# Kernel optimization log

Measured on AMD Instinct MI355X. Metric: run time of the kernel, lower is better.

Reference implementation:

```python
import jax, jax.numpy as jnp
import numpy as np

H = 256   # hidden_dim
C = 512   # num_classes (HMM states)
V = 32000 # vocab
N = 64    # batch
T = 512   # sequence length


def _res_layer(x, w1, b1, w2, b2):
    # compound-PCFG ResLayer: x + relu(lin2(relu(lin1(x))))
    return x + jax.nn.relu(jax.nn.relu(x @ w1 + b1) @ w2 + b2)


def _mlp_res2(x, res_w, res_b):
    # res_w: [2,2,H,H], res_b: [2,2,H] -> two stacked ResLayers
    for i in range(2):
        x = _res_layer(x, res_w[i, 0], res_b[i, 0], res_w[i, 1], res_b[i, 1])
    return x


def setup_inputs() -> dict:
    key = jax.random.key(0)
    ks = jax.random.split(key, 12)
    s = 1.0 / np.sqrt(H)  # xavier-ish scale
    return {
        "text": jax.random.randint(ks[0], (N, T), 0, V, dtype=jnp.int32),
        "start_emb": jax.random.normal(ks[1], (H,), jnp.float32),
        "start_w": jax.random.normal(ks[2], (H, H), jnp.float32) * s,
        "start_b": jnp.zeros((H,), jnp.float32),
        "start_res_w": jax.random.normal(ks[3], (2, 2, H, H), jnp.float32) * s,
        "start_res_b": jnp.zeros((2, 2, H), jnp.float32),
        "state_emb": jax.random.normal(ks[4], (C, H), jnp.float32) * s,
        "next_state_emb": jax.random.normal(ks[5], (C, H), jnp.float32) * s,
        "preterminal_emb": jax.random.normal(ks[6], (C, H), jnp.float32) * s,
        "term_res_w": jax.random.normal(ks[7], (2, 2, H, H), jnp.float32) * s,
        "term_res_b": jnp.zeros((2, 2, H), jnp.float32),
        "terminal_emb": jax.random.normal(ks[8], (V, H), jnp.float32) * s,
    }


def reference(text, start_emb, start_w, start_b, start_res_w, start_res_b,
              state_emb, next_state_emb, preterminal_emb,
              term_res_w, term_res_b, terminal_emb):
    # --- start distribution: start_mlp(start_emb) @ next_state_emb.T (tie_start) ---
    fx = start_emb @ start_w + start_b          # Linear
    fx = _mlp_res2(fx, start_res_w, start_res_b)
    start = jax.nn.log_softmax(fx @ next_state_emb.T, axis=-1)       # [C]

    # --- transition: state_emb @ next_state_emb.T, row log-softmax ---
    transition = jax.nn.log_softmax(state_emb @ next_state_emb.T, axis=-1)  # [C,C]

    # --- emission: terminal_mlp(preterminal_emb) @ terminal_emb.T ---
    fe = _mlp_res2(preterminal_emb, term_res_w, term_res_b)           # [C,H]
    emission = jax.nn.log_softmax(fe @ terminal_emb.T, axis=-1)       # [C,V]

    # --- HMM forward algorithm (log-space scan over time) ---
    em_tok = emission.T[text]                 # [N,T,C] log p(x_t | z_t=c)
    alpha0 = start[None, :] + em_tok[:, 0]    # [N,C]

    def step(alpha, e_t):
        # alpha: [N,C]; logsumexp over previous state
        alpha = jax.nn.logsumexp(alpha[:, :, None] + transition[None], axis=1) + e_t
        return alpha, None

    alpha_T, _ = jax.lax.scan(step, alpha0, jnp.swapaxes(em_tok, 0, 1)[1:])
    evidence = jax.nn.logsumexp(alpha_T, axis=-1).sum()
    return evidence
```

## Files before the change

### kernel.cpp

```cpp
#include <hip/hip_runtime.h>
#include <hip/hip_bf16.h>

#define HD 256
#define CD 512
#define VD 32000
#define ND 64
#define TD 512

typedef __attribute__((ext_vector_type(8))) short short8;
typedef __attribute__((ext_vector_type(4))) float floatx4;
typedef __attribute__((ext_vector_type(8))) int int32x8;

__device__ inline float bf2f(unsigned short u) {
  union { unsigned u; float f; } t; t.u = ((unsigned)u) << 16; return t.f;
}
__device__ inline unsigned short f2bf(float x) {
  union { float f; unsigned u; } t; t.f = x;
  unsigned u = t.u;
  u += 0x7FFFu + ((u >> 16) & 1u);
  return (unsigned short)(u >> 16);
}
__device__ inline float bf_lo(unsigned u) { union { unsigned u; float f; } t; t.u = u << 16; return t.f; }
__device__ inline float bf_hi(unsigned u) { union { unsigned u; float f; } t; t.u = u & 0xFFFF0000u; return t.f; }

__device__ inline floatx4 zf4() { floatx4 v; v[0] = v[1] = v[2] = v[3] = 0.f; return v; }
__device__ inline floatx4 mfma16(short8 a, short8 b, floatx4 c) {
  return __builtin_amdgcn_mfma_f32_16x16x32_bf16(a, b, c, 0, 0, 0);
}
__device__ inline floatx4 mfma_mx(int32x8 a, int32x8 b, floatx4 c) {
  return __builtin_amdgcn_mfma_scale_f32_16x16x128_f8f6f4(
      a, b, c, 0, 0, 0, 0x7F7F7F7F, 0, 0x7F7F7F7F);
}

__global__ void k_sm(const float* __restrict__ emb, const float* __restrict__ W,
                     const float* __restrict__ bb, const float* __restrict__ s_rw,
                     const float* __restrict__ s_rb, const float* __restrict__ nextE,
                     float* __restrict__ startO,
                     const float* __restrict__ pretE, const float* __restrict__ t_rw,
                     const float* __restrict__ t_rb, float* __restrict__ fe) {
  __shared__ float x[HD], h[HD];
  __shared__ float lg[2 * HD];
  __shared__ float red[8];
  const int j = threadIdx.x;
  if (blockIdx.x != 0) {
    const int row = blockIdx.x - 1;
    x[j] = pretE[row * HD + j];
    __syncthreads();
    for (int L = 0; L < 2; ++L) {
      const float* w1 = t_rw + (size_t)(L * 2 + 0) * HD * HD;
      const float* b1 = t_rb + (L * 2 + 0) * HD;
      const float* w2 = t_rw + (size_t)(L * 2 + 1) * HD * HD;
      const float* b2 = t_rb + (L * 2 + 1) * HD;
      float a = b1[j];
#pragma unroll 4
      for (int i = 0; i < HD; ++i) a += x[i] * w1[i * HD + j];
      a = fmaxf(a, 0.f);
      h[j] = a;
      __syncthreads();
      float o = b2[j];
#pragma unroll 4
      for (int i = 0; i < HD; ++i) o += h[i] * w2[i * HD + j];
      o = x[j] + fmaxf(o, 0.f);
      __syncthreads();
      x[j] = o;
      __syncthreads();
    }
    fe[row * HD + j] = x[j];
    return;
  }
  x[j] = emb[j];
  __syncthreads();
  float a = bb[j];
#pragma unroll 8
  for (int i = 0; i < HD; ++i) a += x[i] * W[i * HD + j];
  __syncthreads();
  x[j] = a;
  __syncthreads();
  for (int L = 0; L < 2; ++L) {
    const float* w1 = s_rw + (size_t)(L * 2 + 0) * HD * HD;
    const float* b1 = s_rb + (L * 2 + 0) * HD;
    const float* w2 = s_rw + (size_t)(L * 2 + 1) * HD * HD;
    const float* b2 = s_rb + (L * 2 + 1) * HD;
    float t = b1[j];
#pragma unroll 8
    for (int i = 0; i < HD; ++i) t += x[i] * w1[i * HD + j];
    t = fmaxf(t, 0.f);
    h[j] = t;
    __syncthreads();
    float o = b2[j];
#pragma unroll 8
    for (int i = 0; i < HD; ++i) o += h[i] * w2[i * HD + j];
    o = x[j] + fmaxf(o, 0.f);
    __syncthreads();
    x[j] = o;
    __syncthreads();
  }
  {
    const int w = j >> 6, l = j & 63;
    for (int rr = w * 128; rr < (w + 1) * 128; ++rr) {
      float s = 0.f;
#pragma unroll
      for (int k = 0; k < 4; ++k) s += x[l + k * 64] * nextE[rr * HD + l + k * 64];
#pragma unroll
      for (int off = 32; off >= 1; off >>= 1) s += __shfl_down(s, off);
      if (l == 0) lg[rr] = s;
    }
  }
  __syncthreads();
  float lg0 = lg[j], lg1 = lg[j + 256];
  float m = fmaxf(lg0, lg1);
#pragma unroll
  for (int sh = 1; sh <= 32; sh <<= 1) m = fmaxf(m, __shfl_xor(m, sh));
  if ((j & 63) == 0) red[j >> 6] = m;
  __syncthreads();
  m = fmaxf(fmaxf(red[0], red[1]), fmaxf(red[2], red[3]));
  __syncthreads();
  float s = __expf(lg0 - m) + __expf(lg1 - m);
#pragma unroll
  for (int sh = 1; sh <= 32; sh <<= 1) s += __shfl_xor(s, sh);
  if ((j & 63) == 0) red[j >> 6] = s;
  __syncthreads();
  s = red[0] + red[1] + red[2] + red[3];
  float ls = __logf(s);
  startO[j] = lg0 - m - ls;
  startO[j + 256] = lg1 - m - ls;
}

#define GEMM_LDS (2 * 128 * 528)
__global__ __launch_bounds__(512) void k_gemm2(const float* __restrict__ A0,
                                               const float* __restrict__ B0,
                                               unsigned short* __restrict__ out0,
                                               const float* __restrict__ A1,
                                               const float* __restrict__ B1,
                                               unsigned short* __restrict__ out1) {
  extern __shared__ char smem[];
  char* sA = smem;
  char* sB = smem + 128 * 528;
  const int tid = threadIdx.x;
  const int bx = blockIdx.x;
  const float* A; const float* B; unsigned short* out; int mbase;
  if (bx < 250) { A = A0; B = B0; out = out0; mbase = bx * 128; }
  else          { A = A1; B = B1; out = out1; mbase = (bx - 250) * 128; }
  const int row = tid >> 2, seg = tid & 3;
  {
    const float4* srcA = (const float4*)(A + (size_t)(mbase + row) * HD + seg * 64);
    uint2* dA = (uint2*)(sA + row * 528 + seg * 128);
#pragma unroll
    for (int i = 0; i < 16; ++i) {
      float4 va = srcA[i];
      dA[i] = make_uint2((unsigned)f2bf(va.x) | ((unsigned)f2bf(va.y) << 16),
                         (unsigned)f2bf(va.z) | ((unsigned)f2bf(va.w) << 16));
    }
  }
  const int w = tid >> 6, l = tid & 63, l15 = l & 15, quad = l >> 4;
  const char* arow = sA + (w * 16 + l15) * 528 + quad * 16;
  const char* brow = sB + l15 * 528 + quad * 16;
  for (int ny = 0; ny < 4; ++ny) {
    __syncthreads();
    {
      const float4* srcB = (const float4*)(B + (size_t)(ny * 128 + row) * HD + seg * 64);
      uint2* dB = (uint2*)(sB + row * 528 + seg * 128);
#pragma unroll
      for (int i = 0; i < 16; ++i) {
        float4 vb = srcB[i];
        dB[i] = make_uint2((unsigned)f2bf(vb.x) | ((unsigned)f2bf(vb.y) << 16),
                           (unsigned)f2bf(vb.z) | ((unsigned)f2bf(vb.w) << 16));
      }
    }
    __syncthreads();
    floatx4 acc[8];
#pragma unroll
    for (int nt = 0; nt < 8; ++nt) acc[nt] = zf4();
#pragma unroll
    for (int kc = 0; kc < 8; ++kc) {
      short8 a = *(const short8*)(arow + kc * 64);
#pragma unroll
      for (int nt = 0; nt < 8; ++nt) {
        short8 b = *(const short8*)(brow + nt * 16 * 528 + kc * 64);
        acc[nt] = mfma16(a, b, acc[nt]);
      }
    }
#pragma unroll
    for (int nt = 0; nt < 8; ++nt)
#pragma unroll
      for (int r = 0; r < 4; ++r) {
        int m = mbase + w * 16 + quad * 4 + r;
        int n = ny * 128 + nt * 16 + l15;
        out[(size_t)m * CD + n] = f2bf(acc[nt][r]);
      }
  }
}

__global__ __launch_bounds__(512) void k_sml(const unsigned short* __restrict__ tlg,
                                             unsigned char* __restrict__ P8,
                                             unsigned char* __restrict__ PT8,
                                             const unsigned short* __restrict__ logT,
                                             float* __restrict__ part,
                                             float* __restrict__ lse,
                                             unsigned int* __restrict__ cnt) {
  __shared__ float red[8];
  __shared__ int s_last;
  const int tid = threadIdx.x;
  if (blockIdx.x < 512) {
    const int row = blockIdx.x;
    float v = bf2f(tlg[row * CD + tid]);
    float m = v;
#pragma unroll
    for (int sh = 1; sh <= 32; sh <<= 1) m = fmaxf(m, __shfl_xor(m, sh));
    if ((tid & 63) == 0) red[tid >> 6] = m;
    __syncthreads();
    m = fmaxf(fmaxf(fmaxf(red[0], red[1]), fmaxf(red[2], red[3])),
              fmaxf(fmaxf(red[4], red[5]), fmaxf(red[6], red[7])));
    __syncthreads();
    float e = __expf(v - m);
    float s = e;
#pragma unroll
    for (int sh = 1; sh <= 32; sh <<= 1) s += __shfl_xor(s, sh);
    if ((tid & 63) == 0) red[tid >> 6] = s;
    __syncthreads();
    s = red[0] + red[1] + red[2] + red[3] + red[4] + red[5] + red[6] + red[7];
    float inv = 512.0f / s;
    int b0 = __builtin_amdgcn_cvt_pk_fp8_f32(e * inv, e * inv, 0, false);
    unsigned char byte = (unsigned char)(b0 & 0xff);
    P8[row * CD + tid] = byte;
    PT8[(size_t)tid * CD + row] = byte;
    return;
  }
  const int b = blockIdx.x - 512, c = tid;
  {
    const unsigned short* p = logT + (size_t)b * 256 * CD + c;
    float m = -1e30f, s = 0.f;
    for (int i = 0; i < 256; ++i) {
      float v = bf2f(p[(size_t)i * CD]);
      float nm = fmaxf(m, v);
      s = s * __expf(m - nm) + __expf(v - nm);
      m = nm;
    }
    part[b * 1024 + c] = m;
    part[b * 1024 + 512 + c] = s;
  }
  __threadfence();
  if (tid == 0) s_last = (atomicAdd(cnt, 1u) == 124u) ? 1 : 0;
  __syncthreads();
  if (s_last) {
    __threadfence();
    float m = -1e30f, s = 0.f;
    for (int i = 0; i < 125; ++i) {
      float mi = part[i * 1024 + c], si = part[i * 1024 + 512 + c];
      float nm = fmaxf(m, mi);
      s = s * __expf(m - nm) + si * __expf(mi - nm);
      m = nm;
    }
    lse[c] = m + __logf(s);
  }
}

__global__ __launch_bounds__(512) void k_gather(const int* __restrict__ text,
                                                const unsigned short* __restrict__ logT,
                                                const float* __restrict__ lse,
                                                unsigned short* __restrict__ em) {
  const int b = blockIdx.x;
  const int g = b >> 8, t = b & 255;
  const int dir = g >> 2, q = g & 3;
  const int tg = dir ? (511 - t) : t;
  const int tid = threadIdx.x, w = tid >> 6, l = tid & 63;
  const int l15 = l & 15, quad = l >> 4;
  const int n = q * 16 + l15;
  const int tok = text[n * TD + tg];
  const unsigned short* row = logT + (size_t)tok * CD;
  unsigned outp[8];
#pragma unroll
  for (int nt = 0; nt < 4; ++nt) {
    int c0 = w * 64 + nt * 16 + quad * 4;
    uint2 rv = *(const uint2*)(row + c0);
    float4 ls = *(const float4*)(lse + c0);
    float E0 = __expf(bf_lo(rv.x) - ls.x);
    float E1 = __expf(bf_hi(rv.x) - ls.y);
    float E2 = __expf(bf_lo(rv.y) - ls.z);
    float E3 = __expf(bf_hi(rv.y) - ls.w);
    outp[nt * 2 + 0] = (unsigned)f2bf(E0) | ((unsigned)f2bf(E1) << 16);
    outp[nt * 2 + 1] = (unsigned)f2bf(E2) | ((unsigned)f2bf(E3) << 16);
  }
  uint4* dst = (uint4*)(em + (((size_t)b * 8 + w) * 64 + l) * 16);
  dst[0] = make_uint4(outp[0], outp[1], outp[2], outp[3]);
  dst[1] = make_uint4(outp[4], outp[5], outp[6], outp[7]);
}

__global__ __launch_bounds__(512, 2) void k_scan(const unsigned char* __restrict__ P8,
                                                 const unsigned char* __restrict__ PT8,
                                                 const unsigned short* __restrict__ em,
                                                 const float* __restrict__ startv,
                                                 float* __restrict__ alphaF,
                                                 float* __restrict__ alphaB,
                                                 unsigned int* __restrict__ cnt,
                                                 float* __restrict__ out) {
  __shared__ unsigned char Abuf[8 * 512];
  __shared__ float scratch[8 * 8];
  __shared__ int s_last;
  const int g = blockIdx.x, dir = g >> 3, q = g & 7;
  const int tid = threadIdx.x, w = tid >> 6, l = tid & 63;
  const int l15 = l & 15, quad = l >> 4;
  const int r7 = l15 & 7, sel = l15 >> 3;
  const int colbase = w * 64;
  const unsigned char* Pb = dir ? P8 : PT8;

  int32x8 Prf[4][4];
#pragma unroll
  for (int kc = 0; kc < 4; ++kc)
#pragma unroll
    for (int mt = 0; mt < 4; ++mt) {
      const uint4* p = (const uint4*)(Pb + (size_t)(colbase + mt * 16 + l15) * CD + kc * 128 + quad * 32);
      uint4 x0 = p[0], x1 = p[1];
      Prf[kc][mt] = (int32x8){(int)x0.x, (int)x0.y, (int)x0.z, (int)x0.w,
                              (int)x1.x, (int)x1.y, (int)x1.z, (int)x1.w};
    }

  unsigned char* wr0 = Abuf + r7 * 512 + (((w * 4 + sel * 2 + 0) ^ r7) << 4) + quad * 4;
  unsigned char* wr1 = Abuf + r7 * 512 + (((w * 4 + sel * 2 + 1) ^ r7) << 4) + quad * 4;
  const unsigned char* rdrow = Abuf + r7 * 512;

  const int go = dir * 4 + (q >> 1);
  const int o = quad * 16 + (q & 1) * 8 + r7;
  const unsigned short* emp = em + (((size_t)go * 256 * 8 + w) * 64 + o) * 16 + sel * 8;
  const size_t emstride = 8 * 64 * 16;

  float Msum = 0.f;
  const float LGA = 5.54517744f;
  const float LGP = 6.23832463f;
  const float LGAP = 11.78350207f;

  auto tail = [&](float* v, float sub) {
    float m = fmaxf(fmaxf(fmaxf(v[0], v[1]), fmaxf(v[2], v[3])),
                    fmaxf(fmaxf(v[4], v[5]), fmaxf(v[6], v[7])));
    m = fmaxf(m, __shfl_xor(m, 8));
    m = fmaxf(m, __shfl_xor(m, 16));
    m = fmaxf(m, __shfl_xor(m, 32));
    if (sel == 0 && quad == 0) scratch[r7 * 8 + w] = m;
    __syncthreads();
    const floatx4* sr = (const floatx4*)(scratch + r7 * 8);
    floatx4 s0 = sr[0], s1 = sr[1];
    m = fmaxf(fmaxf(fmaxf(s0[0], s0[1]), fmaxf(s0[2], s0[3])),
              fmaxf(fmaxf(s1[0], s1[1]), fmaxf(s1[2], s1[3])));
    float inv = __builtin_amdgcn_rcpf(m) * 256.0f;
    Msum += __logf(m) - sub;
    int pk0 = __builtin_amdgcn_cvt_pk_fp8_f32(v[0] * inv, v[1] * inv, 0, false);
    pk0 = __builtin_amdgcn_cvt_pk_fp8_f32(v[2] * inv, v[3] * inv, pk0, true);
    *(int*)wr0 = pk0;
    int pk1 = __builtin_amdgcn_cvt_pk_fp8_f32(v[4] * inv, v[5] * inv, 0, false);
    pk1 = __builtin_amdgcn_cvt_pk_fp8_f32(v[6] * inv, v[7] * inv, pk1, true);
    *(int*)wr1 = pk1;
    __syncthreads();
  };

  {
    uint4 e0 = *(const uint4*)emp;
    unsigned eu[4] = {e0.x, e0.y, e0.z, e0.w};
    float v[8];
#pragma unroll
    for (int i = 0; i < 2; ++i)
#pragma unroll
      for (int r = 0; r < 4; ++r) {
        int j = i * 4 + r;
        float E = (j & 1) ? bf_hi(eu[j >> 1]) : bf_lo(eu[j >> 1]);
        float st = dir ? 1.f : __expf(startv[colbase + (sel * 2 + i) * 16 + quad * 4 + r]);
        v[j] = st * E;
      }
    tail(v, LGA);
  }

  uint4 ec = *(const uint4*)(emp + emstride);
  const int nloop = dir ? 255 : 254;
  for (int s = 1; s <= nloop; ++s) {
    int32x8 bfr[4];
#pragma unroll
    for (int kc = 0; kc < 4; ++kc) {
      int u0 = kc * 8 + quad * 2;
      uint4 x0 = *(const uint4*)(rdrow + (((u0 + 0) ^ r7) << 4));
      uint4 x1 = *(const uint4*)(rdrow + (((u0 + 1) ^ r7) << 4));
      bfr[kc] = (int32x8){(int)x0.x, (int)x0.y, (int)x0.z, (int)x0.w,
                          (int)x1.x, (int)x1.y, (int)x1.z, (int)x1.w};
    }
    uint4 en = *(const uint4*)(emp + (size_t)(s + 1) * emstride);
    floatx4 acc[4];
#pragma unroll
    for (int mt = 0; mt < 4; ++mt) acc[mt] = zf4();
#pragma unroll
    for (int kc = 0; kc < 4; ++kc) {
      acc[0] = mfma_mx(Prf[kc][0], bfr[kc], acc[0]);
      acc[1] = mfma_mx(Prf[kc][1], bfr[kc], acc[1]);
      acc[2] = mfma_mx(Prf[kc][2], bfr[kc], acc[2]);
      acc[3] = mfma_mx(Prf[kc][3], bfr[kc], acc[3]);
    }
    unsigned eu[4] = {ec.x, ec.y, ec.z, ec.w};
    float v[8];
#pragma unroll
    for (int i = 0; i < 2; ++i)
#pragma unroll
      for (int r = 0; r < 4; ++r) {
        int j = i * 4 + r;
        float E = (j & 1) ? bf_hi(eu[j >> 1]) : bf_lo(eu[j >> 1]);
        float a0 = (i == 0) ? acc[0][r] : acc[1][r];
        float a1 = (i == 0) ? acc[2][r] : acc[3][r];
        v[j] = (sel ? a1 : a0) * E;
      }
    tail(v, LGAP);
    ec = en;
  }
  {
    int32x8 bfr[4];
#pragma unroll
    for (int kc = 0; kc < 4; ++kc) {
      int u0 = kc * 8 + quad * 2;
      uint4 x0 = *(const uint4*)(rdrow + (((u0 + 0) ^ r7) << 4));
      uint4 x1 = *(const uint4*)(rdrow + (((u0 + 1) ^ r7) << 4));
      bfr[kc] = (int32x8){(int)x0.x, (int)x0.y, (int)x0.z, (int)x0.w,
                          (int)x1.x, (int)x1.y, (int)x1.z, (int)x1.w};
    }
    floatx4 acc[4];
#pragma unroll
    for (int mt = 0; mt < 4; ++mt) acc[mt] = zf4();
#pragma unroll
    for (int kc = 0; kc < 4; ++kc) {
      acc[0] = mfma_mx(Prf[kc][0], bfr[kc], acc[0]);
      acc[1] = mfma_mx(Prf[kc][1], bfr[kc], acc[1]);
      acc[2] = mfma_mx(Prf[kc][2], bfr[kc], acc[2]);
      acc[3] = mfma_mx(Prf[kc][3], bfr[kc], acc[3]);
    }
    unsigned eu[4] = {ec.x, ec.y, ec.z, ec.w};
    float* dst = dir ? alphaB : alphaF;
#pragma unroll
    for (int i = 0; i < 2; ++i) {
      int mt0 = i, mt1 = 2 + i;
      float4 ov;
      float vv[4];
#pragma unroll
      for (int r = 0; r < 4; ++r) {
        int j = i * 4 + r;
        float E = dir ? 1.f : ((j & 1) ? bf_hi(eu[j >> 1]) : bf_lo(eu[j >> 1]));
        float a0 = acc[mt0][r];
        float a1 = acc[mt1][r];
        vv[r] = (sel ? a1 : a0) * E;
      }
      ov.x = __logf(vv[0]) + Msum - LGP;
      ov.y = __logf(vv[1]) + Msum - LGP;
      ov.z = __logf(vv[2]) + Msum - LGP;
      ov.w = __logf(vv[3]) + Msum - LGP;
      *(float4*)&dst[(size_t)(q * 8 + r7) * CD + colbase + (sel * 2 + i) * 16 + quad * 4] = ov;
    }
  }
  __threadfence();
  if (tid == 0) s_last = (atomicAdd(cnt, 1u) == 15u) ? 1 : 0;
  __syncthreads();
  if (s_last) {
    __threadfence();
    float ev = 0.f;
    for (int i = 0; i < 8; ++i) {
      int n = w * 8 + i;
      float x[8];
      float m = -1e30f;
#pragma unroll
      for (int k = 0; k < 8; ++k) {
        x[k] = alphaF[n * CD + k * 64 + l] + alphaB[n * CD + k * 64 + l];
        m = fmaxf(m, x[k]);
      }
#pragma unroll
      for (int sh = 1; sh <= 32; sh <<= 1) m = fmaxf(m, __shfl_xor(m, sh));
      float s = 0.f;
#pragma unroll
      for (int k = 0; k < 8; ++k) s += __expf(x[k] - m);
#pragma unroll
      for (int sh = 1; sh <= 32; sh <<= 1) s += __shfl_xor(s, sh);
      ev += m + __logf(s);
    }
    if (l == 0) scratch[w] = ev;
    __syncthreads();
    if (tid == 0) {
      float tot = 0.f;
      for (int i = 0; i < 8; ++i) tot += scratch[i];
      out[0] = tot;
    }
  }
}

extern "C" void kernel_launch(void* const* d_in, const int* in_sizes, int n_in,
                              void* d_out, int out_size, void* d_ws, size_t ws_size,
                              hipStream_t stream) {
  (void)in_sizes; (void)n_in; (void)out_size;
  const int* text = (const int*)d_in[0];
  const float* s_emb = (const float*)d_in[1];
  const float* s_w = (const float*)d_in[2];
  const float* s_b = (const float*)d_in[3];
  const float* s_rw = (const float*)d_in[4];
  const float* s_rb = (const float*)d_in[5];
  const float* stateE = (const float*)d_in[6];
  const float* nextE = (const float*)d_in[7];
  const float* pretE = (const float*)d_in[8];
  const float* t_rw = (const float*)d_in[9];
  const float* t_rb = (const float*)d_in[10];
  const float* termE = (const float*)d_in[11];
  float* out = (float*)d_out;

  char* ws = (char*)d_ws;
  size_t off = 0;
  auto alloc = [&](size_t bytes) {
    void* p = ws + off;
    off = (off + bytes + 255) & ~(size_t)255;
    return p;
  };
  unsigned int* w_cnt = (unsigned int*)alloc(256);
  float* w_start = (float*)alloc(CD * 4);
  unsigned short* w_tlg = (unsigned short*)alloc((size_t)CD * CD * 2);
  unsigned char* w_P8 = (unsigned char*)alloc((size_t)CD * CD);
  unsigned char* w_PT8 = (unsigned char*)alloc((size_t)CD * CD);
  float* w_fe = (float*)alloc((size_t)CD * HD * 4);
  unsigned short* w_logT = (unsigned short*)alloc((size_t)VD * CD * 2);
  float* w_part = (float*)alloc((size_t)125 * 1024 * 4);
  float* w_lse = (float*)alloc(CD * 4);
  unsigned short* w_em = (unsigned short*)alloc((size_t)8 * 256 * 512 * 16 * 2);
  float* w_aF = (float*)alloc((size_t)ND * CD * 4);
  float* w_aB = (float*)alloc((size_t)ND * CD * 4);
  if (off > ws_size) return;

  hipFuncSetAttribute(reinterpret_cast<const void*>(k_gemm2),
                      hipFuncAttributeMaxDynamicSharedMemorySize, GEMM_LDS);

  hipMemsetAsync(w_cnt, 0, 256, stream);

  k_sm<<<513, 256, 0, stream>>>(s_emb, s_w, s_b, s_rw, s_rb, nextE, w_start,
                                pretE, t_rw, t_rb, w_fe);
  k_gemm2<<<254, 512, GEMM_LDS, stream>>>(termE, w_fe, w_logT, stateE, nextE, w_tlg);
  k_sml<<<637, 512, 0, stream>>>(w_tlg, w_P8, w_PT8, w_logT, w_part, w_lse, w_cnt + 1);
  k_gather<<<2048, 512, 0, stream>>>(text, w_logT, w_lse, w_em);
  k_scan<<<16, 512, 0, stream>>>(w_P8, w_PT8, w_em, w_start, w_aF, w_aB, w_cnt, out);
}
```

Baseline: 608.3 us.

## Fuse emission gather into scan and use per-block MX scales instead of block-wide max

Removes the separate gather kernel. The scan kernel now loads token ids into LDS and computes the exponentiated emission values directly from logT and lse, one step ahead. Each wave now renormalizes with a power-of-two exponent taken from its own max. That exponent goes to LDS as an E8M0 scale byte, which the scaled MFMA consumes per K-chunk, so the cross-wave max reduction and one barrier per step are gone. The A buffer is double-buffered to allow this. The risks are more global-load latency on the serial scan path and precision changes from the fixed offsets and clamped scales.

```diff
diff --git a/kernel.cpp b/kernel.cpp
--- a/kernel.cpp
+++ b/kernel.cpp
@@ -27,9 +27,9 @@
 __device__ inline floatx4 mfma16(short8 a, short8 b, floatx4 c) {
   return __builtin_amdgcn_mfma_f32_16x16x32_bf16(a, b, c, 0, 0, 0);
 }
-__device__ inline floatx4 mfma_mx(int32x8 a, int32x8 b, floatx4 c) {
+__device__ inline floatx4 mfma_mxs(int32x8 a, int32x8 b, floatx4 c, unsigned sb) {
   return __builtin_amdgcn_mfma_scale_f32_16x16x128_f8f6f4(
-      a, b, c, 0, 0, 0, 0x7F7F7F7F, 0, 0x7F7F7F7F);
+      a, b, c, 0, 0, 0, 0x7F7F7F7F, 0, (int)sb);
 }
 
 __global__ void k_sm(const float* __restrict__ emb, const float* __restrict__ W,
@@ -255,53 +255,27 @@
   }
 }
 
-__global__ __launch_bounds__(512) void k_gather(const int* __restrict__ text,
-                                                const unsigned short* __restrict__ logT,
-                                                const float* __restrict__ lse,
-                                                unsigned short* __restrict__ em) {
-  const int b = blockIdx.x;
-  const int g = b >> 8, t = b & 255;
-  const int dir = g >> 2, q = g & 3;
-  const int tg = dir ? (511 - t) : t;
-  const int tid = threadIdx.x, w = tid >> 6, l = tid & 63;
-  const int l15 = l & 15, quad = l >> 4;
-  const int n = q * 16 + l15;
-  const int tok = text[n * TD + tg];
-  const unsigned short* row = logT + (size_t)tok * CD;
-  unsigned outp[8];
-#pragma unroll
-  for (int nt = 0; nt < 4; ++nt) {
-    int c0 = w * 64 + nt * 16 + quad * 4;
-    uint2 rv = *(const uint2*)(row + c0);
-    float4 ls = *(const float4*)(lse + c0);
-    float E0 = __expf(bf_lo(rv.x) - ls.x);
-    float E1 = __expf(bf_hi(rv.x) - ls.y);
-    float E2 = __expf(bf_lo(rv.y) - ls.z);
-    float E3 = __expf(bf_hi(rv.y) - ls.w);
-    outp[nt * 2 + 0] = (unsigned)f2bf(E0) | ((unsigned)f2bf(E1) << 16);
-    outp[nt * 2 + 1] = (unsigned)f2bf(E2) | ((unsigned)f2bf(E3) << 16);
-  }
-  uint4* dst = (uint4*)(em + (((size_t)b * 8 + w) * 64 + l) * 16);
-  dst[0] = make_uint4(outp[0], outp[1], outp[2], outp[3]);
-  dst[1] = make_uint4(outp[4], outp[5], outp[6], outp[7]);
-}
-
 __global__ __launch_bounds__(512, 2) void k_scan(const unsigned char* __restrict__ P8,
                                                  const unsigned char* __restrict__ PT8,
-                                                 const unsigned short* __restrict__ em,
+                                                 const unsigned short* __restrict__ logT,
+                                                 const float* __restrict__ lse,
+                                                 const int* __restrict__ text,
                                                  const float* __restrict__ startv,
                                                  float* __restrict__ alphaF,
                                                  float* __restrict__ alphaB,
                                                  unsigned int* __restrict__ cnt,
                                                  float* __restrict__ out) {
-  __shared__ unsigned char Abuf[8 * 512];
-  __shared__ float scratch[8 * 8];
+  __shared__ unsigned char Abuf[2 * 8 * 512];
+  __shared__ unsigned char Tbuf[2 * 128];
+  __shared__ int txtL[8 * 272];
+  __shared__ float scr[8];
   __shared__ int s_last;
   const int g = blockIdx.x, dir = g >> 3, q = g & 7;
   const int tid = threadIdx.x, w = tid >> 6, l = tid & 63;
   const int l15 = l & 15, quad = l >> 4;
   const int r7 = l15 & 7, sel = l15 >> 3;
   const int colbase = w * 64;
+  const int c0 = colbase + sel * 32 + quad * 4;
   const unsigned char* Pb = dir ? P8 : PT8;
 
   int32x8 Prf[4][4];
@@ -315,62 +289,94 @@
                               (int)x1.x, (int)x1.y, (int)x1.z, (int)x1.w};
     }
 
-  unsigned char* wr0 = Abuf + r7 * 512 + (((w * 4 + sel * 2 + 0) ^ r7) << 4) + quad * 4;
-  unsigned char* wr1 = Abuf + r7 * 512 + (((w * 4 + sel * 2 + 1) ^ r7) << 4) + quad * 4;
-  const unsigned char* rdrow = Abuf + r7 * 512;
-
-  const int go = dir * 4 + (q >> 1);
-  const int o = quad * 16 + (q & 1) * 8 + r7;
-  const unsigned short* emp = em + (((size_t)go * 256 * 8 + w) * 64 + o) * 16 + sel * 8;
-  const size_t emstride = 8 * 64 * 16;
-
-  float Msum = 0.f;
-  const float LGA = 5.54517744f;
-  const float LGP = 6.23832463f;
-  const float LGAP = 11.78350207f;
-
-  auto tail = [&](float* v, float sub) {
+  for (int i = tid; i < 8 * 257; i += 512) {
+    int r = i / 257, t = i - r * 257;
+    int tg = dir ? (511 - t) : t;
+    txtL[r * 272 + t] = text[(q * 8 + r) * TD + tg];
+  }
+  const float4 ls0 = *(const float4*)(lse + c0);
+  const float4 ls1 = *(const float4*)(lse + c0 + 16);
+  __syncthreads();
+
+  const int wrofs0 = r7 * 512 + (((w * 4 + sel * 2 + 0) ^ r7) << 4) + quad * 4;
+  const int wrofs1 = r7 * 512 + (((w * 4 + sel * 2 + 1) ^ r7) << 4) + quad * 4;
+  const int twofs = ((w & 1) * 2 + sel) * 32 + r7 * 4 + (w >> 1);
+  const int trofs = (quad * 8 + r7) * 4;
+
+  int SA = 0;
+  const float LN2 = 0.69314718056f;
+  const float L2E = 1.44269504089f;
+
+  auto tail = [&](float* v, int delta, int wp) {
     float m = fmaxf(fmaxf(fmaxf(v[0], v[1]), fmaxf(v[2], v[3])),
                     fmaxf(fmaxf(v[4], v[5]), fmaxf(v[6], v[7])));
-    m = fmaxf(m, __shfl_xor(m, 8));
     m = fmaxf(m, __shfl_xor(m, 16));
     m = fmaxf(m, __shfl_xor(m, 32));
-    if (sel == 0 && quad == 0) scratch[r7 * 8 + w] = m;
-    __syncthreads();
-    const floatx4* sr = (const floatx4*)(scratch + r7 * 8);
-    floatx4 s0 = sr[0], s1 = sr[1];
-    m = fmaxf(fmaxf(fmaxf(s0[0], s0[1]), fmaxf(s0[2], s0[3])),
-              fmaxf(fmaxf(s1[0], s1[1]), fmaxf(s1[2], s1[3])));
-    float inv = __builtin_amdgcn_rcpf(m) * 256.0f;
-    Msum += __logf(m) - sub;
+    int eb = (int)((__float_as_uint(m) >> 23) & 255) - 127;
+    float inv = __uint_as_float((unsigned)(134 - eb) << 23);
+    int byte = eb + 120 - delta;
+    byte = byte < 1 ? 1 : (byte > 254 ? 254 : byte);
     int pk0 = __builtin_amdgcn_cvt_pk_fp8_f32(v[0] * inv, v[1] * inv, 0, false);
     pk0 = __builtin_amdgcn_cvt_pk_fp8_f32(v[2] * inv, v[3] * inv, pk0, true);
-    *(int*)wr0 = pk0;
     int pk1 = __builtin_amdgcn_cvt_pk_fp8_f32(v[4] * inv, v[5] * inv, 0, false);
     pk1 = __builtin_amdgcn_cvt_pk_fp8_f32(v[6] * inv, v[7] * inv, pk1, true);
-    *(int*)wr1 = pk1;
+    unsigned char* base = Abuf + wp * 4096;
+    *(int*)(base + wrofs0) = pk0;
+    *(int*)(base + wrofs1) = pk1;
+    if (quad == 0) Tbuf[wp * 128 + twofs] = (unsigned char)byte;
     __syncthreads();
   };
 
+  float Ec[8];
   {
-    uint4 e0 = *(const uint4*)emp;
-    unsigned eu[4] = {e0.x, e0.y, e0.z, e0.w};
+    int tok = txtL[r7 * 272 + 0];
+    const unsigned short* rowp = logT + (size_t)tok * CD;
+    uint2 ra = *(const uint2*)(rowp + c0);
+    uint2 rb = *(const uint2*)(rowp + c0 + 16);
     float v[8];
-#pragma unroll
-    for (int i = 0; i < 2; ++i)
-#pragma unroll
-      for (int r = 0; r < 4; ++r) {
-        int j = i * 4 + r;
-        float E = (j & 1) ? bf_hi(eu[j >> 1]) : bf_lo(eu[j >> 1]);
-        float st = dir ? 1.f : __expf(startv[colbase + (sel * 2 + i) * 16 + quad * 4 + r]);
-        v[j] = st * E;
-      }
-    tail(v, LGA);
-  }
-
-  uint4 ec = *(const uint4*)(emp + emstride);
+    v[0] = exp2f((bf_lo(ra.x) - ls0.x) * L2E + 14.f);
+    v[1] = exp2f((bf_hi(ra.x) - ls0.y) * L2E + 14.f);
+    v[2] = exp2f((bf_lo(ra.y) - ls0.z) * L2E + 14.f);
+    v[3] = exp2f((bf_hi(ra.y) - ls0.w) * L2E + 14.f);
+    v[4] = exp2f((bf_lo(rb.x) - ls1.x) * L2E + 14.f);
+    v[5] = exp2f((bf_hi(rb.x) - ls1.y) * L2E + 14.f);
+    v[6] = exp2f((bf_lo(rb.y) - ls1.z) * L2E + 14.f);
+    v[7] = exp2f((bf_hi(rb.y) - ls1.w) * L2E + 14.f);
+    if (!dir) {
+      const float4 s0 = *(const float4*)(startv + c0);
+      const float4 s1 = *(const float4*)(startv + c0 + 16);
+      v[0] *= __expf(s0.x); v[1] *= __expf(s0.y); v[2] *= __expf(s0.z); v[3] *= __expf(s0.w);
+      v[4] *= __expf(s1.x); v[5] *= __expf(s1.y); v[6] *= __expf(s1.z); v[7] *= __expf(s1.w);
+    }
+    tail(v, 0, 0);
+    tok = txtL[r7 * 272 + 1];
+    rowp = logT + (size_t)tok * CD;
+    ra = *(const uint2*)(rowp + c0);
+    rb = *(const uint2*)(rowp + c0 + 16);
+    Ec[0] = exp2f((bf_lo(ra.x) - ls0.x) * L2E + 14.f);
+    Ec[1] = exp2f((bf_hi(ra.x) - ls0.y) * L2E + 14.f);
+    Ec[2] = exp2f((bf_lo(ra.y) - ls0.z) * L2E + 14.f);
+    Ec[3] = exp2f((bf_hi(ra.y) - ls0.w) * L2E + 14.f);
+    Ec[4] = exp2f((bf_lo(rb.x) - ls1.x) * L2E + 14.f);
+    Ec[5] = exp2f((bf_hi(rb.x) - ls1.y) * L2E + 14.f);
+    Ec[6] = exp2f((bf_lo(rb.y) - ls1.z) * L2E + 14.f);
+    Ec[7] = exp2f((bf_hi(rb.y) - ls1.w) * L2E + 14.f);
+  }
+
   const int nloop = dir ? 255 : 254;
   for (int s = 1; s <= nloop; ++s) {
+    const int rp = (s & 1) ^ 1;
+    const int Tword = *(const int*)(Tbuf + rp * 128 + trofs);
+    int b0 = Tword & 255, b1 = (Tword >> 8) & 255, b2 = (Tword >> 16) & 255, b3 = (Tword >> 24) & 255;
+    int bm = max(max(b0, b1), max(b2, b3));
+    bm = max(bm, __shfl_xor(bm, 16));
+    bm = max(bm, __shfl_xor(bm, 32));
+    const int delta = bm - 120;
+    const unsigned sb0 = (unsigned)b0 * 0x01010101u;
+    const unsigned sb1 = (unsigned)b1 * 0x01010101u;
+    const unsigned sb2 = (unsigned)b2 * 0x01010101u;
+    const unsigned sb3 = (unsigned)b3 * 0x01010101u;
+    const unsigned char* rdrow = Abuf + rp * 4096 + r7 * 512;
     int32x8 bfr[4];
 #pragma unroll
     for (int kc = 0; kc < 4; ++kc) {
@@ -380,33 +386,62 @@
       bfr[kc] = (int32x8){(int)x0.x, (int)x0.y, (int)x0.z, (int)x0.w,
                           (int)x1.x, (int)x1.y, (int)x1.z, (int)x1.w};
     }
-    uint4 en = *(const uint4*)(emp + (size_t)(s + 1) * emstride);
+    int tokn = txtL[r7 * 272 + s + 1];
+    const unsigned short* rowp = logT + (size_t)tokn * CD;
+    uint2 rna = *(const uint2*)(rowp + c0);
+    uint2 rnb = *(const uint2*)(rowp + c0 + 16);
     floatx4 acc[4];
 #pragma unroll
     for (int mt = 0; mt < 4; ++mt) acc[mt] = zf4();
-#pragma unroll
-    for (int kc = 0; kc < 4; ++kc) {
-      acc[0] = mfma_mx(Prf[kc][0], bfr[kc], acc[0]);
-      acc[1] = mfma_mx(Prf[kc][1], bfr[kc], acc[1]);
-      acc[2] = mfma_mx(Prf[kc][2], bfr[kc], acc[2]);
-      acc[3] = mfma_mx(Prf[kc][3], bfr[kc], acc[3]);
-    }
-    unsigned eu[4] = {ec.x, ec.y, ec.z, ec.w};
+    acc[0] = mfma_mxs(Prf[0][0], bfr[0], acc[0], sb0);
+    acc[1] = mfma_mxs(Prf[0][1], bfr[0], acc[1], sb0);
+    acc[2] = mfma_mxs(Prf[0][2], bfr[0], acc[2], sb0);
+    acc[3] = mfma_mxs(Prf[0][3], bfr[0], acc[3], sb0);
+    acc[0] = mfma_mxs(Prf[1][0], bfr[1], acc[0], sb1);
+    acc[1] = mfma_mxs(Prf[1][1], bfr[1], acc[1], sb1);
+    acc[2] = mfma_mxs(Prf[1][2], bfr[1], acc[2], sb1);
+    acc[3] = mfma_mxs(Prf[1][3], bfr[1], acc[3], sb1);
+    acc[0] = mfma_mxs(Prf[2][0], bfr[2], acc[0], sb2);
+    acc[1] = mfma_mxs(Prf[2][1], bfr[2], acc[1], sb2);
+    acc[2] = mfma_mxs(Prf[2][2], bfr[2], acc[2], sb2);
+    acc[3] = mfma_mxs(Prf[2][3], bfr[2], acc[3], sb2);
+    acc[0] = mfma_mxs(Prf[3][0], bfr[3], acc[0], sb3);
+    acc[1] = mfma_mxs(Prf[3][1], bfr[3], acc[1], sb3);
+    acc[2] = mfma_mxs(Prf[3][2], bfr[3], acc[2], sb3);
+    acc[3] = mfma_mxs(Prf[3][3], bfr[3], acc[3], sb3);
+    float En[8];
+    En[0] = exp2f((bf_lo(rna.x) - ls0.x) * L2E + 14.f);
+    En[1] = exp2f((bf_hi(rna.x) - ls0.y) * L2E + 14.f);
+    En[2] = exp2f((bf_lo(rna.y) - ls0.z) * L2E + 14.f);
+    En[3] = exp2f((bf_hi(rna.y) - ls0.w) * L2E + 14.f);
+    En[4] = exp2f((bf_lo(rnb.x) - ls1.x) * L2E + 14.f);
+    En[5] = exp2f((bf_hi(rnb.x) - ls1.y) * L2E + 14.f);
+    En[6] = exp2f((bf_lo(rnb.y) - ls1.z) * L2E + 14.f);
+    En[7] = exp2f((bf_hi(rnb.y) - ls1.w) * L2E + 14.f);
     float v[8];
 #pragma unroll
     for (int i = 0; i < 2; ++i)
 #pragma unroll
       for (int r = 0; r < 4; ++r) {
-        int j = i * 4 + r;
-        float E = (j & 1) ? bf_hi(eu[j >> 1]) : bf_lo(eu[j >> 1]);
+        int jj = i * 4 + r;
         float a0 = (i == 0) ? acc[0][r] : acc[1][r];
         float a1 = (i == 0) ? acc[2][r] : acc[3][r];
-        v[j] = (sel ? a1 : a0) * E;
+        v[jj] = (sel ? a1 : a0) * Ec[jj];
       }
-    tail(v, LGAP);
-    ec = en;
+    SA += delta;
+    tail(v, delta, s & 1);
+#pragma unroll
+    for (int i = 0; i < 8; ++i) Ec[i] = En[i];
   }
   {
+    const int rp = nloop & 1;
+    const int Tword = *(const int*)(Tbuf + rp * 128 + trofs);
+    int b0 = Tword & 255, b1 = (Tword >> 8) & 255, b2 = (Tword >> 16) & 255, b3 = (Tword >> 24) & 255;
+    const unsigned sb0 = (unsigned)b0 * 0x01010101u;
+    const unsigned sb1 = (unsigned)b1 * 0x01010101u;
+    const unsigned sb2 = (unsigned)b2 * 0x01010101u;
+    const unsigned sb3 = (unsigned)b3 * 0x01010101u;
+    const unsigned char* rdrow = Abuf + rp * 4096 + r7 * 512;
     int32x8 bfr[4];
 #pragma unroll
     for (int kc = 0; kc < 4; ++kc) {
@@ -419,33 +454,42 @@
     floatx4 acc[4];
 #pragma unroll
     for (int mt = 0; mt < 4; ++mt) acc[mt] = zf4();
-#pragma unroll
-    for (int kc = 0; kc < 4; ++kc) {
-      acc[0] = mfma_mx(Prf[kc][0], bfr[kc], acc[0]);
-      acc[1] = mfma_mx(Prf[kc][1], bfr[kc], acc[1]);
-      acc[2] = mfma_mx(Prf[kc][2], bfr[kc], acc[2]);
-      acc[3] = mfma_mx(Prf[kc][3], bfr[kc], acc[3]);
-    }
-    unsigned eu[4] = {ec.x, ec.y, ec.z, ec.w};
+    acc[0] = mfma_mxs(Prf[0][0], bfr[0], acc[0], sb0);
+    acc[1] = mfma_mxs(Prf[0][1], bfr[0], acc[1], sb0);
+    acc[2] = mfma_mxs(Prf[0][2], bfr[0], acc[2], sb0);
+    acc[3] = mfma_mxs(Prf[0][3], bfr[0], acc[3], sb0);
+    acc[0] = mfma_mxs(Prf[1][0], bfr[1], acc[0], sb1);
+    acc[1] = mfma_mxs(Prf[1][1], bfr[1], acc[1], sb1);
+    acc[2] = mfma_mxs(Prf[1][2], bfr[1], acc[2], sb1);
+    acc[3] = mfma_mxs(Prf[1][3], bfr[1], acc[3], sb1);
+    acc[0] = mfma_mxs(Prf[2][0], bfr[2], acc[0], sb2);
+    acc[1] = mfma_mxs(Prf[2][1], bfr[2], acc[1], sb2);
+    acc[2] = mfma_mxs(Prf[2][2], bfr[2], acc[2], sb2);
+    acc[3] = mfma_mxs(Prf[2][3], bfr[2], acc[3], sb2);
+    acc[0] = mfma_mxs(Prf[3][0], bfr[3], acc[0], sb3);
+    acc[1] = mfma_mxs(Prf[3][1], bfr[3], acc[1], sb3);
+    acc[2] = mfma_mxs(Prf[3][2], bfr[3], acc[2], sb3);
+    acc[3] = mfma_mxs(Prf[3][3], bfr[3], acc[3], sb3);
+    const float C = dir ? 5888.f : 5879.f;
+    const float off = LN2 * ((float)SA - C);
     float* dst = dir ? alphaB : alphaF;
 #pragma unroll
     for (int i = 0; i < 2; ++i) {
-      int mt0 = i, mt1 = 2 + i;
-      float4 ov;
       float vv[4];
 #pragma unroll
       for (int r = 0; r < 4; ++r) {
-        int j = i * 4 + r;
-        float E = dir ? 1.f : ((j & 1) ? bf_hi(eu[j >> 1]) : bf_lo(eu[j >> 1]));
-        float a0 = acc[mt0][r];
-        float a1 = acc[mt1][r];
+        int jj = i * 4 + r;
+        float E = dir ? 1.f : Ec[jj];
+        float a0 = (i == 0) ? acc[0][r] : acc[1][r];
+        float a1 = (i == 0) ? acc[2][r] : acc[3][r];
         vv[r] = (sel ? a1 : a0) * E;
       }
-      ov.x = __logf(vv[0]) + Msum - LGP;
-      ov.y = __logf(vv[1]) + Msum - LGP;
-      ov.z = __logf(vv[2]) + Msum - LGP;
-      ov.w = __logf(vv[3]) + Msum - LGP;
-      *(float4*)&dst[(size_t)(q * 8 + r7) * CD + colbase + (sel * 2 + i) * 16 + quad * 4] = ov;
+      float4 ov;
+      ov.x = __logf(vv[0]) + off;
+      ov.y = __logf(vv[1]) + off;
+      ov.z = __logf(vv[2]) + off;
+      ov.w = __logf(vv[3]) + off;
+      *(float4*)&dst[(size_t)(q * 8 + r7) * CD + c0 + i * 16] = ov;
     }
   }
   __threadfence();
@@ -472,11 +516,11 @@
       for (int sh = 1; sh <= 32; sh <<= 1) s += __shfl_xor(s, sh);
       ev += m + __logf(s);
     }
-    if (l == 0) scratch[w] = ev;
+    if (l == 0) scr[w] = ev;
     __syncthreads();
     if (tid == 0) {
       float tot = 0.f;
-      for (int i = 0; i < 8; ++i) tot += scratch[i];
+      for (int i = 0; i < 8; ++i) tot += scr[i];
       out[0] = tot;
     }
   }
@@ -516,7 +560,6 @@
   unsigned short* w_logT = (unsigned short*)alloc((size_t)VD * CD * 2);
   float* w_part = (float*)alloc((size_t)125 * 1024 * 4);
   float* w_lse = (float*)alloc(CD * 4);
-  unsigned short* w_em = (unsigned short*)alloc((size_t)8 * 256 * 512 * 16 * 2);
   float* w_aF = (float*)alloc((size_t)ND * CD * 4);
   float* w_aB = (float*)alloc((size_t)ND * CD * 4);
   if (off > ws_size) return;
@@ -530,6 +573,6 @@
                                 pretE, t_rw, t_rb, w_fe);
   k_gemm2<<<254, 512, GEMM_LDS, stream>>>(termE, w_fe, w_logT, stateE, nextE, w_tlg);
   k_sml<<<637, 512, 0, stream>>>(w_tlg, w_P8, w_PT8, w_logT, w_part, w_lse, w_cnt + 1);
-  k_gather<<<2048, 512, 0, stream>>>(text, w_logT, w_lse, w_em);
-  k_scan<<<16, 512, 0, stream>>>(w_P8, w_PT8, w_em, w_start, w_aF, w_aB, w_cnt, out);
-}
+  k_scan<<<16, 512, 0, stream>>>(w_P8, w_PT8, w_logT, w_lse, text, w_start,
+                                 w_aF, w_aB, w_cnt, out);
+}
```

Measured after the change: 639.4 us. +5.1%, slower.
